# Performance work log

Measured on AMD Instinct MI355X. Metric: run time of the kernel, lower is better.

## Reference

```python
import jax, jax.numpy as jnp
import numpy as np

N_NODES = 100000
N_EDGES = 1600000
DIM = 64
N_GRAPHS = 1000


def setup_inputs() -> dict:
    key = jax.random.key(0)
    ks = jax.random.split(key, 6)
    s = 1.0 / np.sqrt(DIM)
    x = jax.random.normal(ks[0], (N_NODES, DIM), dtype=jnp.float32)
    edge_index = jax.random.randint(ks[1], (2, N_EDGES), 0, N_NODES, dtype=jnp.int64)
    batch = jnp.sort(jax.random.randint(ks[2], (N_NODES,), 0, N_GRAPHS, dtype=jnp.int64))
    W1 = jax.random.normal(ks[3], (DIM, DIM), dtype=jnp.float32) * s
    b1 = jnp.zeros((DIM,), jnp.float32)
    W2 = jax.random.normal(ks[4], (DIM, DIM), dtype=jnp.float32) * s
    b2 = jnp.zeros((DIM,), jnp.float32)
    return {"x": x, "W1": W1, "b1": b1, "W2": W2, "b2": b2,
            "edge_index": edge_index, "batch": batch}


def reference(x, W1, b1, W2, b2, edge_index, batch):
    n = x.shape[0]
    loop = jnp.arange(n, dtype=edge_index.dtype)
    src = jnp.concatenate([edge_index[0], loop])  # [E+N] with self-loops
    dst = jnp.concatenate([edge_index[1], loop])
    # symmetric GCN normalization: deg^{-1/2}[src] * deg^{-1/2}[dst]
    deg = jax.ops.segment_sum(jnp.ones(src.shape[0], x.dtype), dst, num_segments=n)
    dinv = jax.lax.rsqrt(jnp.maximum(deg, 1.0))  # deg >= 1 due to self-loops
    norm = (dinv[src] * dinv[dst])[:, None]      # [E+N, 1]

    def gcn(h, W, b):
        h = h @ W                                  # transform first (smaller dim path)
        msg = h[src] * norm                        # gather + normalize
        return jax.ops.segment_sum(msg, dst, num_segments=n) + b

    h = jax.nn.relu(gcn(x, W1, b1))
    # dropout: eval mode -> identity
    h = jax.nn.relu(gcn(h, W2, b2))

    counts = jax.ops.segment_sum(jnp.ones((n,), x.dtype), batch, num_segments=N_GRAPHS)
    pooled = jax.ops.segment_sum(h, batch, num_segments=N_GRAPHS)
    return pooled / jnp.maximum(counts, 1.0)[:, None]
```

## Files before the change

kernel.cpp:

```cpp
#include <hip/hip_runtime.h>
#include <hip/hip_fp16.h>

#define DIM 64
#define BIN_SHIFT 7
#define BINSZ 128
#define MAXBINS 1024
#define PB 512
#define PB_LOG 9

typedef __attribute__((ext_vector_type(2))) float floatx2;
typedef __attribute__((ext_vector_type(4))) float f32x4;
typedef __attribute__((ext_vector_type(8))) _Float16 f16x8;
typedef __attribute__((ext_vector_type(4))) _Float16 f16x4;

__device__ __forceinline__ int slice_of(int bid) {
    return ((bid & 7) << 6) | (bid >> 3);
}

__device__ __forceinline__ void scan_bsums(const int* __restrict__ bsums, int nb2,
                                           int* __restrict__ bp) {
    int t = threadIdx.x;
    if (t < 64) {
        int a = (t < nb2) ? bsums[t] : 0;
        int b = (64 + t < nb2) ? bsums[64 + t] : 0;
        int A = a, B = b;
#pragma unroll
        for (int d = 1; d < 64; d <<= 1) {
            int ta = __shfl_up(A, d); if (t >= d) A += ta;
            int tb = __shfl_up(B, d); if (t >= d) B += tb;
        }
        int Ta = __shfl(A, 63);
        bp[t] = A - a;
        bp[64 + t] = Ta + B - b;
    }
}


__global__ __launch_bounds__(256) void k_hist(const int* __restrict__ dst,
                                              int* __restrict__ C, int E, int NB) {
    __shared__ int h[MAXBINS];
    for (int i = threadIdx.x; i < NB; i += 256) h[i] = 0;
    __syncthreads();
    int blk = slice_of(blockIdx.x);
    int per = (E + PB - 1) / PB;
    int e0 = blk * per;
    int e1 = e0 + per; if (e1 > E) e1 = E;
    for (int e = e0 + (int)threadIdx.x; e < e1; e += 256)
        atomicAdd(&h[dst[e] >> BIN_SHIFT], 1);
    __syncthreads();
    for (int i = threadIdx.x; i < NB; i += 256)
        C[i * PB + blk] = h[i];
}


__global__ __launch_bounds__(1024) void k_scanA(const int* __restrict__ C,
                                                int* __restrict__ S,
                                                int* __restrict__ bsums, int M) {
    __shared__ int sh[1024];
    int tid = threadIdx.x;
    int j0 = blockIdx.x * 4096 + tid * 4;
    int v[4]; int sum = 0;
#pragma unroll
    for (int t = 0; t < 4; ++t) {
        int j = j0 + t;
        int x = (j < M) ? C[j] : 0;
        v[t] = sum; sum += x;
    }
    sh[tid] = sum;
    __syncthreads();
#pragma unroll
    for (int d = 1; d < 1024; d <<= 1) {
        int t = (tid >= d) ? sh[tid - d] : 0;
        __syncthreads();
        sh[tid] += t;
        __syncthreads();
    }
    int excl = sh[tid] - sum;
#pragma unroll
    for (int t = 0; t < 4; ++t) {
        int j = j0 + t;
        if (j < M) S[j] = excl + v[t];
    }
    if (tid == 1023) bsums[blockIdx.x] = sh[1023];
}


__global__ __launch_bounds__(256) void k_bucket(const int* __restrict__ src,
                                                const int* __restrict__ dst,
                                                const int* __restrict__ S,
                                                const int* __restrict__ bsums,
                                                int* __restrict__ bkt, int E, int NB,
                                                int nb2) {
    __shared__ int lcur[MAXBINS];
    __shared__ int bp[128];
    scan_bsums(bsums, nb2, bp);
    int blk = slice_of(blockIdx.x);
    __syncthreads();
    for (int i = threadIdx.x; i < NB; i += 256) {
        int j = i * PB + blk;
        lcur[i] = S[j] + bp[j >> 12];
    }
    __syncthreads();
    int per = (E + PB - 1) / PB;
    int e0 = blk * per;
    int e1 = e0 + per; if (e1 > E) e1 = E;
    for (int e = e0 + (int)threadIdx.x; e < e1; e += 256) {
        int d = dst[e];
        int pos = atomicAdd(&lcur[d >> BIN_SHIFT], 1);
        bkt[pos] = src[e] | ((d & (BINSZ - 1)) << 24);
    }
}


__global__ __launch_bounds__(256) void k_binsort(const int* __restrict__ bkt,
                                                 const int* __restrict__ S,
                                                 const int* __restrict__ bsums,
                                                 int* __restrict__ csr,
                                                 int* __restrict__ off,
                                                 float* __restrict__ dinv,
                                                 const int* __restrict__ batch,
                                                 int* __restrict__ goff,
                                                 float* __restrict__ outz,
                                                 int N, int G, int E, int NB, int nb2) {
    __shared__ int cnt[BINSZ], bas[BINSZ], cur[BINSZ];
    __shared__ int wsum[4];
    __shared__ int bp[128];
    int tid = threadIdx.x;
    int b = blockIdx.x;
    scan_bsums(bsums, nb2, bp);
    if (tid < BINSZ) { cnt[tid] = 0; cur[tid] = 0; }
    for (int i = b * 256 + tid; i < G * DIM; i += NB * 256) outz[i] = 0.f;
    __syncthreads();
    int j0 = b << PB_LOG;
    int s0 = S[j0] + bp[j0 >> 12];
    int s1 = E;
    if (b + 1 < NB) { int j1 = (b + 1) << PB_LOG; s1 = S[j1] + bp[j1 >> 12]; }
    for (int i = s0 + tid; i < s1; i += 256)
        atomicAdd(&cnt[(bkt[i] >> 24) & (BINSZ - 1)], 1);
    __syncthreads();
    int my = (tid < BINSZ) ? cnt[tid] : 0;
    int lane = tid & 63, wv = tid >> 6;
    int x = my;
#pragma unroll
    for (int d = 1; d < 64; d <<= 1) {
        int t = __shfl_up(x, d);
        if (lane >= d) x += t;
    }
    if (lane == 63) wsum[wv] = x;
    __syncthreads();
    int prefix = 0;
    for (int w = 0; w < wv; ++w) prefix += wsum[w];
    int ex = x + prefix - my;
    if (tid < BINSZ) {
        bas[tid] = ex;
        int v = (b << BIN_SHIFT) + tid;
        if (v < N) {
            off[v] = s0 + ex;
            dinv[v] = rsqrtf((float)(my + 1));
            if (v == N - 1) off[N] = E;
            int bb = batch[v];
            int prev = (v == 0) ? -1 : batch[v - 1];
            for (int g = prev + 1; g <= bb; ++g) goff[g] = v;
            if (v == N - 1)
                for (int g = bb + 1; g <= G; ++g) goff[g] = N;
        }
    }
    __syncthreads();
    for (int i = s0 + tid; i < s1; i += 256) {
        int p = bkt[i];
        int lo = (p >> 24) & (BINSZ - 1);
        int li = atomicAdd(&cur[lo], 1);
        csr[s0 + bas[lo] + li] = p & 0xFFFFFF;
    }
}


__global__ __launch_bounds__(256) void k_gemm(const float* __restrict__ X,
                                              const float* __restrict__ W,
                                              const float* __restrict__ dinv,
                                              unsigned int* __restrict__ Y8, int N) {
    __shared__ float Os[16 * 68];
    int tid = threadIdx.x;
    int lane = tid & 63, w = tid >> 6;
    int m = lane & 15, g = lane >> 4;
    int row0 = blockIdx.x * 16;
    int row = row0 + m;

    f16x8 B0, B1;
    {
        int n = (w << 4) + m;
        const float* wp = W + (g << 3) * 64 + n;
#pragma unroll
        for (int j = 0; j < 8; ++j) B0[j] = (_Float16)wp[j * 64];
        wp += 32 * 64;
#pragma unroll
        for (int j = 0; j < 8; ++j) B1[j] = (_Float16)wp[j * 64];
    }
    f16x8 A0, A1;
    {
        float4 u0 = make_float4(0.f, 0.f, 0.f, 0.f), u1 = u0, u2 = u0, u3 = u0;
        if (row < N) {
            const float* xp = X + (size_t)row * DIM + (g << 3);
            u0 = *(const float4*)(xp);
            u1 = *(const float4*)(xp + 4);
            u2 = *(const float4*)(xp + 32);
            u3 = *(const float4*)(xp + 36);
        }
        A0[0] = (_Float16)u0.x; A0[1] = (_Float16)u0.y; A0[2] = (_Float16)u0.z; A0[3] = (_Float16)u0.w;
        A0[4] = (_Float16)u1.x; A0[5] = (_Float16)u1.y; A0[6] = (_Float16)u1.z; A0[7] = (_Float16)u1.w;
        A1[0] = (_Float16)u2.x; A1[1] = (_Float16)u2.y; A1[2] = (_Float16)u2.z; A1[3] = (_Float16)u2.w;
        A1[4] = (_Float16)u3.x; A1[5] = (_Float16)u3.y; A1[6] = (_Float16)u3.z; A1[7] = (_Float16)u3.w;
    }
    f32x4 acc = {0.f, 0.f, 0.f, 0.f};
    acc = __builtin_amdgcn_mfma_f32_16x16x32_f16(A0, B0, acc, 0, 0, 0);
    acc = __builtin_amdgcn_mfma_f32_16x16x32_f16(A1, B1, acc, 0, 0, 0);
#pragma unroll
    for (int j = 0; j < 4; ++j)
        Os[((g << 2) + j) * 68 + (w << 4) + m] = acc[j];
    __syncthreads();

    int r = tid >> 4, c = tid & 15;
    int orow = row0 + r;
    if (orow < N) {
        float4 o = *(const float4*)(Os + r * 68 + (c << 2));
        float s = dinv[orow];
        int p = 0;
        p = __builtin_amdgcn_cvt_pk_fp8_f32(o.x * s, o.y * s, p, false);
        p = __builtin_amdgcn_cvt_pk_fp8_f32(o.z * s, o.w * s, p, true);
        Y8[(size_t)orow * 16 + c] = (unsigned int)p;
    } else if (orow == N) {
        Y8[(size_t)orow * 16 + c] = 0u;
    }
}


__device__ __forceinline__ float4 gather_rows(const unsigned int* __restrict__ hs8,
                                              const int* __restrict__ csr,
                                              int k0, int k1, int v, int l, int gw4,
                                              int N) {
    float4 a0, a1, a2, a3;
    {
        unsigned int u = hs8[(unsigned)((v << 4) | l)];
        floatx2 f0 = __builtin_amdgcn_cvt_pk_f32_fp8((int)u, false);
        floatx2 f1 = __builtin_amdgcn_cvt_pk_f32_fp8((int)u, true);
        a0 = make_float4(f0.x, f0.y, f1.x, f1.y);
        a1 = make_float4(0.f, 0.f, 0.f, 0.f);
        a2 = make_float4(0.f, 0.f, 0.f, 0.f);
        a3 = make_float4(0.f, 0.f, 0.f, 0.f);
    }
    for (int kb = k0; kb < k1; kb += 16) {
        int rem = k1 - kb;
        int idx = (l < rem) ? csr[kb + l] : N;
        unsigned uu[16];
#pragma unroll
        for (int t = 0; t < 16; ++t) {
            int s = __shfl(idx, gw4 + t);
            uu[t] = hs8[(unsigned)((s << 4) | l)];
        }
#pragma unroll
        for (int t = 0; t < 16; t += 4) {
            floatx2 q0 = __builtin_amdgcn_cvt_pk_f32_fp8((int)uu[t + 0], false);
            floatx2 q1 = __builtin_amdgcn_cvt_pk_f32_fp8((int)uu[t + 0], true);
            floatx2 q2 = __builtin_amdgcn_cvt_pk_f32_fp8((int)uu[t + 1], false);
            floatx2 q3 = __builtin_amdgcn_cvt_pk_f32_fp8((int)uu[t + 1], true);
            floatx2 q4 = __builtin_amdgcn_cvt_pk_f32_fp8((int)uu[t + 2], false);
            floatx2 q5 = __builtin_amdgcn_cvt_pk_f32_fp8((int)uu[t + 2], true);
            floatx2 q6 = __builtin_amdgcn_cvt_pk_f32_fp8((int)uu[t + 3], false);
            floatx2 q7 = __builtin_amdgcn_cvt_pk_f32_fp8((int)uu[t + 3], true);
            a0.x += q0.x; a0.y += q0.y; a0.z += q1.x; a0.w += q1.y;
            a1.x += q2.x; a1.y += q2.y; a1.z += q3.x; a1.w += q3.y;
            a2.x += q4.x; a2.y += q4.y; a2.z += q5.x; a2.w += q5.y;
            a3.x += q6.x; a3.y += q6.y; a3.z += q7.x; a3.w += q7.y;
        }
    }
    return make_float4(a0.x + a1.x + a2.x + a3.x,
                       a0.y + a1.y + a2.y + a3.y,
                       a0.z + a1.z + a2.z + a3.z,
                       a0.w + a1.w + a2.w + a3.w);
}


__global__ __launch_bounds__(256) void k_gather_gemm(const unsigned int* __restrict__ hs8,
                                                     const int* __restrict__ csr,
                                                     const int* __restrict__ off,
                                                     const float* __restrict__ dinv,
                                                     const float* __restrict__ bias,
                                                     const float* __restrict__ W,
                                                     unsigned int* __restrict__ hs_out,
                                                     int N) {
    __shared__ _Float16 Xs[16 * 72];
    __shared__ float Os[16 * 68];
    int tid = threadIdx.x;
    int r = tid >> 4, l = tid & 15;
    int lane = tid & 63, w = tid >> 6;
    int m = lane & 15, g = lane >> 4;
    int gw4 = (r & 3) << 4;
    int v = blockIdx.x * 16 + r;

    f16x8 B0, B1;
    {
        int n = (w << 4) + m;
        const float* wp = W + (g << 3) * 64 + n;
#pragma unroll
        for (int j = 0; j < 8; ++j) B0[j] = (_Float16)wp[j * 64];
        wp += 32 * 64;
#pragma unroll
        for (int j = 0; j < 8; ++j) B1[j] = (_Float16)wp[j * 64];
    }
    if (blockIdx.x == 0 && tid < 16)
        hs_out[(size_t)N * 16 + tid] = 0u;

    float dv = 0.f;
    float4 h = make_float4(0.f, 0.f, 0.f, 0.f);
    if (v < N) {
        dv = dinv[v];
        float4 bv = ((const float4*)bias)[l];
        float4 acc = gather_rows(hs8, csr, off[v], off[v + 1], v, l, gw4, N);
        h.x = fmaxf(acc.x * dv + bv.x, 0.f);
        h.y = fmaxf(acc.y * dv + bv.y, 0.f);
        h.z = fmaxf(acc.z * dv + bv.z, 0.f);
        h.w = fmaxf(acc.w * dv + bv.w, 0.f);
    }
    {
        f16x4 hv;
        hv[0] = (_Float16)h.x; hv[1] = (_Float16)h.y;
        hv[2] = (_Float16)h.z; hv[3] = (_Float16)h.w;
        *(f16x4*)(Xs + r * 72 + (l << 2)) = hv;
    }
    __syncthreads();

    f16x8 A0 = *(const f16x8*)(Xs + m * 72 + (g << 3));
    f16x8 A1 = *(const f16x8*)(Xs + m * 72 + 32 + (g << 3));
    f32x4 acc2 = {0.f, 0.f, 0.f, 0.f};
    acc2 = __builtin_amdgcn_mfma_f32_16x16x32_f16(A0, B0, acc2, 0, 0, 0);
    acc2 = __builtin_amdgcn_mfma_f32_16x16x32_f16(A1, B1, acc2, 0, 0, 0);
#pragma unroll
    for (int j = 0; j < 4; ++j)
        Os[((g << 2) + j) * 68 + (w << 4) + m] = acc2[j];
    __syncthreads();

    if (v < N) {
        float4 o = *(const float4*)(Os + r * 68 + (l << 2));
        int p = 0;
        p = __builtin_amdgcn_cvt_pk_fp8_f32(o.x * dv, o.y * dv, p, false);
        p = __builtin_amdgcn_cvt_pk_fp8_f32(o.z * dv, o.w * dv, p, true);
        hs_out[(size_t)v * 16 + l] = (unsigned int)p;
    }
}


__global__ __launch_bounds__(256) void k_gather_pool(const unsigned int* __restrict__ hs8,
                                                     const int* __restrict__ csr,
                                                     const int* __restrict__ off,
                                                     const float* __restrict__ dinv,
                                                     const float* __restrict__ bias,
                                                     const int* __restrict__ batch,
                                                     const int* __restrict__ goff,
                                                     float* __restrict__ out, int N) {
    __shared__ float vals[16][68];
    __shared__ int gid[16];
    int tid = threadIdx.x;
    int r = tid >> 4, l = tid & 15;
    int gw4 = (r & 3) << 4;
    int v = blockIdx.x * 16 + r;

    float4 val = make_float4(0.f, 0.f, 0.f, 0.f);
    int g = -1;
    if (v < N) {
        g = batch[v];
        float dv = dinv[v];
        float4 bv = ((const float4*)bias)[l];
        float4 acc = gather_rows(hs8, csr, off[v], off[v + 1], v, l, gw4, N);
        float inv = 1.0f / (float)(goff[g + 1] - goff[g]);
        val.x = fmaxf(acc.x * dv + bv.x, 0.f) * inv;
        val.y = fmaxf(acc.y * dv + bv.y, 0.f) * inv;
        val.z = fmaxf(acc.z * dv + bv.z, 0.f) * inv;
        val.w = fmaxf(acc.w * dv + bv.w, 0.f) * inv;
    }
    *(float4*)(&vals[r][l << 2]) = val;
    if (l == 0) gid[r] = g;
    __syncthreads();

    if (v < N) {
        bool leader = (r == 0) || (gid[r - 1] != g);
        if (leader) {
            float4 sacc = val;
            for (int rr = r + 1; rr < 16 && gid[rr] == g; ++rr) {
                float4 t = *(const float4*)(&vals[rr][l << 2]);
                sacc.x += t.x; sacc.y += t.y; sacc.z += t.z; sacc.w += t.w;
            }
            float* op = out + (size_t)g * DIM + (l << 2);
            atomicAdd(op + 0, sacc.x);
            atomicAdd(op + 1, sacc.y);
            atomicAdd(op + 2, sacc.z);
            atomicAdd(op + 3, sacc.w);
        }
    }
}


static inline int cdiv(int a, int b) { return (a + b - 1) / b; }

extern "C" void kernel_launch(void* const* d_in, const int* in_sizes, int n_in,
                              void* d_out, int out_size, void* d_ws, size_t ws_size,
                              hipStream_t stream) {
    const float* x   = (const float*)d_in[0];
    const float* W1  = (const float*)d_in[1];
    const float* b1  = (const float*)d_in[2];
    const float* W2  = (const float*)d_in[3];
    const float* b2  = (const float*)d_in[4];
    const int*   ei  = (const int*)d_in[5];
    const int*   bat = (const int*)d_in[6];

    const int N = in_sizes[0] / DIM;
    const int E = in_sizes[5] / 2;
    const int G = out_size / DIM;
    const int NB = cdiv(N, BINSZ);
    const int M  = NB * PB;
    const int* src = ei;
    const int* dst = ei + E;
    float* out = (float*)d_out;

    __half* hs1    = (__half*)d_ws;
    __half* hs2    = hs1 + (size_t)(N + 1) * DIM;
    float*  dinv   = (float*)(hs2 + (size_t)(N + 1) * DIM);
    int*    off    = (int*)(dinv + N);
    int*    goff   = off + (N + 1);
    int*    C      = goff + (G + 1);
    int*    S      = C + (size_t)PB * NB;
    int*    bsums  = S + (size_t)PB * NB;
    int*    csr    = bsums + 1024;
    int*    bkt    = (int*)hs1;

    int nb2 = cdiv(M, 4096);

    k_hist<<<PB, 256, 0, stream>>>(dst, C, E, NB);
    k_scanA<<<nb2, 1024, 0, stream>>>(C, S, bsums, M);
    k_bucket<<<PB, 256, 0, stream>>>(src, dst, S, bsums, bkt, E, NB, nb2);
    k_binsort<<<NB, 256, 0, stream>>>(bkt, S, bsums, csr, off, dinv, bat, goff,
                                      out, N, G, E, NB, nb2);

    k_gemm<<<cdiv(N + 1, 16), 256, 0, stream>>>(x, W1, dinv, (unsigned int*)hs1, N);

    k_gather_gemm<<<cdiv(N, 16), 256, 0, stream>>>((const unsigned int*)hs1, csr, off,
                                                   dinv, b1, W2, (unsigned int*)hs2, N);

    k_gather_pool<<<cdiv(N, 16), 256, 0, stream>>>((const unsigned int*)hs2, csr, off,
                                                   dinv, b2, bat, goff, out, N);
}
```

Baseline: 187.6 us.

## Fuse CSR preprocessing kernels into one cooperative kernel with grid syncs

Merges the histogram, scan, bucket and bin-sort kernels into a single cooperative kernel of 512 blocks that uses grid-wide barriers between phases. The scan is re-chunked to 1024 elements per block so the block sums fit in a 512-entry local scan, and the bin-sort phase loops over bins with a grid-stride. This removes three kernel launch gaps. In exchange it pays grid-sync overhead, and the bin-sort phase now runs on 512 persistent blocks instead of one block per bin.

```diff
diff --git a/kernel.cpp b/kernel.cpp
--- a/kernel.cpp
+++ b/kernel.cpp
@@ -1,5 +1,8 @@
 #include <hip/hip_runtime.h>
 #include <hip/hip_fp16.h>
+#include <hip/hip_cooperative_groups.h>
+
+namespace cg = cooperative_groups;
 
 #define DIM 64
 #define BIN_SHIFT 7
@@ -17,160 +20,147 @@
     return ((bid & 7) << 6) | (bid >> 3);
 }
 
-__device__ __forceinline__ void scan_bsums(const int* __restrict__ bsums, int nb2,
-                                           int* __restrict__ bp) {
-    int t = threadIdx.x;
-    if (t < 64) {
-        int a = (t < nb2) ? bsums[t] : 0;
-        int b = (64 + t < nb2) ? bsums[64 + t] : 0;
-        int A = a, B = b;
-#pragma unroll
-        for (int d = 1; d < 64; d <<= 1) {
-            int ta = __shfl_up(A, d); if (t >= d) A += ta;
-            int tb = __shfl_up(B, d); if (t >= d) B += tb;
-        }
-        int Ta = __shfl(A, 63);
-        bp[t] = A - a;
-        bp[64 + t] = Ta + B - b;
-    }
-}
-
-
-__global__ __launch_bounds__(256) void k_hist(const int* __restrict__ dst,
-                                              int* __restrict__ C, int E, int NB) {
-    __shared__ int h[MAXBINS];
-    for (int i = threadIdx.x; i < NB; i += 256) h[i] = 0;
-    __syncthreads();
-    int blk = slice_of(blockIdx.x);
+
+__global__ __launch_bounds__(256, 2) void k_pre(const int* __restrict__ src,
+                                                const int* __restrict__ dst,
+                                                int* __restrict__ C,
+                                                int* __restrict__ S,
+                                                int* __restrict__ bsums,
+                                                int* __restrict__ bkt,
+                                                int* __restrict__ csr,
+                                                int* __restrict__ off,
+                                                float* __restrict__ dinv,
+                                                const int* __restrict__ batch,
+                                                int* __restrict__ goff,
+                                                float* __restrict__ outz,
+                                                int N, int G, int E, int NB, int nch) {
+    cg::grid_group grid = cg::this_grid();
+    __shared__ int sh[MAXBINS];
+    __shared__ int bp[512];
+    __shared__ int wsum[4];
+    int tid = threadIdx.x;
+    int bid = blockIdx.x;
+    int blk = slice_of(bid);
     int per = (E + PB - 1) / PB;
     int e0 = blk * per;
     int e1 = e0 + per; if (e1 > E) e1 = E;
-    for (int e = e0 + (int)threadIdx.x; e < e1; e += 256)
-        atomicAdd(&h[dst[e] >> BIN_SHIFT], 1);
-    __syncthreads();
-    for (int i = threadIdx.x; i < NB; i += 256)
-        C[i * PB + blk] = h[i];
-}
-
-
-__global__ __launch_bounds__(1024) void k_scanA(const int* __restrict__ C,
-                                                int* __restrict__ S,
-                                                int* __restrict__ bsums, int M) {
-    __shared__ int sh[1024];
-    int tid = threadIdx.x;
-    int j0 = blockIdx.x * 4096 + tid * 4;
-    int v[4]; int sum = 0;
-#pragma unroll
-    for (int t = 0; t < 4; ++t) {
-        int j = j0 + t;
-        int x = (j < M) ? C[j] : 0;
-        v[t] = sum; sum += x;
-    }
-    sh[tid] = sum;
-    __syncthreads();
-#pragma unroll
-    for (int d = 1; d < 1024; d <<= 1) {
-        int t = (tid >= d) ? sh[tid - d] : 0;
-        __syncthreads();
-        sh[tid] += t;
-        __syncthreads();
-    }
-    int excl = sh[tid] - sum;
-#pragma unroll
-    for (int t = 0; t < 4; ++t) {
-        int j = j0 + t;
-        if (j < M) S[j] = excl + v[t];
-    }
-    if (tid == 1023) bsums[blockIdx.x] = sh[1023];
-}
-
-
-__global__ __launch_bounds__(256) void k_bucket(const int* __restrict__ src,
-                                                const int* __restrict__ dst,
-                                                const int* __restrict__ S,
-                                                const int* __restrict__ bsums,
-                                                int* __restrict__ bkt, int E, int NB,
-                                                int nb2) {
-    __shared__ int lcur[MAXBINS];
-    __shared__ int bp[128];
-    scan_bsums(bsums, nb2, bp);
-    int blk = slice_of(blockIdx.x);
-    __syncthreads();
-    for (int i = threadIdx.x; i < NB; i += 256) {
+    int M = NB * PB;
+
+    for (int i = tid; i < NB; i += 256) sh[i] = 0;
+    __syncthreads();
+    for (int e = e0 + tid; e < e1; e += 256)
+        atomicAdd(&sh[dst[e] >> BIN_SHIFT], 1);
+    __syncthreads();
+    for (int i = tid; i < NB; i += 256)
+        C[i * PB + blk] = sh[i];
+    for (int i = bid * 256 + tid; i < G * DIM; i += PB * 256) outz[i] = 0.f;
+    grid.sync();
+
+    if (bid < nch) {
+        int j0 = bid * 1024 + tid * 4;
+        int v[4]; int sum = 0;
+#pragma unroll
+        for (int t = 0; t < 4; ++t) {
+            int j = j0 + t;
+            int x = (j < M) ? C[j] : 0;
+            v[t] = sum; sum += x;
+        }
+        sh[tid] = sum;
+        __syncthreads();
+#pragma unroll
+        for (int d = 1; d < 256; d <<= 1) {
+            int t = (tid >= d) ? sh[tid - d] : 0;
+            __syncthreads();
+            sh[tid] += t;
+            __syncthreads();
+        }
+        int excl = sh[tid] - sum;
+#pragma unroll
+        for (int t = 0; t < 4; ++t) {
+            int j = j0 + t;
+            if (j < M) S[j] = excl + v[t];
+        }
+        if (tid == 255) bsums[bid] = sh[255];
+    }
+    grid.sync();
+
+    if (tid < 64) {
+        int v8[8]; int s = 0;
+#pragma unroll
+        for (int k = 0; k < 8; ++k) {
+            int j = tid * 8 + k;
+            v8[k] = s;
+            s += (j < nch) ? bsums[j] : 0;
+        }
+        int x = s;
+#pragma unroll
+        for (int d = 1; d < 64; d <<= 1) {
+            int t = __shfl_up(x, d);
+            if (tid >= d) x += t;
+        }
+        int base = x - s;
+#pragma unroll
+        for (int k = 0; k < 8; ++k) bp[tid * 8 + k] = base + v8[k];
+    }
+    __syncthreads();
+    for (int i = tid; i < NB; i += 256) {
         int j = i * PB + blk;
-        lcur[i] = S[j] + bp[j >> 12];
-    }
-    __syncthreads();
-    int per = (E + PB - 1) / PB;
-    int e0 = blk * per;
-    int e1 = e0 + per; if (e1 > E) e1 = E;
-    for (int e = e0 + (int)threadIdx.x; e < e1; e += 256) {
+        sh[i] = S[j] + bp[j >> 10];
+    }
+    __syncthreads();
+    for (int e = e0 + tid; e < e1; e += 256) {
         int d = dst[e];
-        int pos = atomicAdd(&lcur[d >> BIN_SHIFT], 1);
+        int pos = atomicAdd(&sh[d >> BIN_SHIFT], 1);
         bkt[pos] = src[e] | ((d & (BINSZ - 1)) << 24);
     }
-}
-
-
-__global__ __launch_bounds__(256) void k_binsort(const int* __restrict__ bkt,
-                                                 const int* __restrict__ S,
-                                                 const int* __restrict__ bsums,
-                                                 int* __restrict__ csr,
-                                                 int* __restrict__ off,
-                                                 float* __restrict__ dinv,
-                                                 const int* __restrict__ batch,
-                                                 int* __restrict__ goff,
-                                                 float* __restrict__ outz,
-                                                 int N, int G, int E, int NB, int nb2) {
-    __shared__ int cnt[BINSZ], bas[BINSZ], cur[BINSZ];
-    __shared__ int wsum[4];
-    __shared__ int bp[128];
-    int tid = threadIdx.x;
-    int b = blockIdx.x;
-    scan_bsums(bsums, nb2, bp);
-    if (tid < BINSZ) { cnt[tid] = 0; cur[tid] = 0; }
-    for (int i = b * 256 + tid; i < G * DIM; i += NB * 256) outz[i] = 0.f;
-    __syncthreads();
-    int j0 = b << PB_LOG;
-    int s0 = S[j0] + bp[j0 >> 12];
-    int s1 = E;
-    if (b + 1 < NB) { int j1 = (b + 1) << PB_LOG; s1 = S[j1] + bp[j1 >> 12]; }
-    for (int i = s0 + tid; i < s1; i += 256)
-        atomicAdd(&cnt[(bkt[i] >> 24) & (BINSZ - 1)], 1);
-    __syncthreads();
-    int my = (tid < BINSZ) ? cnt[tid] : 0;
-    int lane = tid & 63, wv = tid >> 6;
-    int x = my;
-#pragma unroll
-    for (int d = 1; d < 64; d <<= 1) {
-        int t = __shfl_up(x, d);
-        if (lane >= d) x += t;
-    }
-    if (lane == 63) wsum[wv] = x;
-    __syncthreads();
-    int prefix = 0;
-    for (int w = 0; w < wv; ++w) prefix += wsum[w];
-    int ex = x + prefix - my;
-    if (tid < BINSZ) {
-        bas[tid] = ex;
-        int v = (b << BIN_SHIFT) + tid;
-        if (v < N) {
-            off[v] = s0 + ex;
-            dinv[v] = rsqrtf((float)(my + 1));
-            if (v == N - 1) off[N] = E;
-            int bb = batch[v];
-            int prev = (v == 0) ? -1 : batch[v - 1];
-            for (int g = prev + 1; g <= bb; ++g) goff[g] = v;
-            if (v == N - 1)
-                for (int g = bb + 1; g <= G; ++g) goff[g] = N;
-        }
-    }
-    __syncthreads();
-    for (int i = s0 + tid; i < s1; i += 256) {
-        int p = bkt[i];
-        int lo = (p >> 24) & (BINSZ - 1);
-        int li = atomicAdd(&cur[lo], 1);
-        csr[s0 + bas[lo] + li] = p & 0xFFFFFF;
+    grid.sync();
+
+    int* cnt = sh; int* bas = sh + 128; int* cur = sh + 256;
+    for (int b = bid; b < NB; b += PB) {
+        int j0b = b << PB_LOG;
+        int s0 = S[j0b] + bp[j0b >> 10];
+        int s1 = E;
+        if (b + 1 < NB) { int j1 = (b + 1) << PB_LOG; s1 = S[j1] + bp[j1 >> 10]; }
+        if (tid < BINSZ) { cnt[tid] = 0; cur[tid] = 0; }
+        __syncthreads();
+        for (int i = s0 + tid; i < s1; i += 256)
+            atomicAdd(&cnt[(bkt[i] >> 24) & (BINSZ - 1)], 1);
+        __syncthreads();
+        int my = (tid < BINSZ) ? cnt[tid] : 0;
+        int lane = tid & 63, wv = tid >> 6;
+        int x = my;
+#pragma unroll
+        for (int d = 1; d < 64; d <<= 1) {
+            int t = __shfl_up(x, d);
+            if (lane >= d) x += t;
+        }
+        if (lane == 63) wsum[wv] = x;
+        __syncthreads();
+        int prefix = 0;
+        for (int w = 0; w < wv; ++w) prefix += wsum[w];
+        int ex = x + prefix - my;
+        if (tid < BINSZ) {
+            bas[tid] = ex;
+            int v = (b << BIN_SHIFT) + tid;
+            if (v < N) {
+                off[v] = s0 + ex;
+                dinv[v] = rsqrtf((float)(my + 1));
+                if (v == N - 1) off[N] = E;
+                int bb = batch[v];
+                int prev = (v == 0) ? -1 : batch[v - 1];
+                for (int g = prev + 1; g <= bb; ++g) goff[g] = v;
+                if (v == N - 1)
+                    for (int g = bb + 1; g <= G; ++g) goff[g] = N;
+            }
+        }
+        __syncthreads();
+        for (int i = s0 + tid; i < s1; i += 256) {
+            int p = bkt[i];
+            int lo = (p >> 24) & (BINSZ - 1);
+            int li = atomicAdd(&cur[lo], 1);
+            csr[s0 + bas[lo] + li] = p & 0xFFFFFF;
+        }
+        __syncthreads();
     }
 }
 
@@ -432,13 +422,16 @@
     int*    csr    = bsums + 1024;
     int*    bkt    = (int*)hs1;
 
-    int nb2 = cdiv(M, 4096);
-
-    k_hist<<<PB, 256, 0, stream>>>(dst, C, E, NB);
-    k_scanA<<<nb2, 1024, 0, stream>>>(C, S, bsums, M);
-    k_bucket<<<PB, 256, 0, stream>>>(src, dst, S, bsums, bkt, E, NB, nb2);
-    k_binsort<<<NB, 256, 0, stream>>>(bkt, S, bsums, csr, off, dinv, bat, goff,
-                                      out, N, G, E, NB, nb2);
+    int nch = (M + 1023) >> 10;
+
+    {
+        int N_ = N, G_ = G, E_ = E, NB_ = NB, nch_ = nch;
+        void* args[] = {(void*)&src, (void*)&dst, (void*)&C, (void*)&S,
+                        (void*)&bsums, (void*)&bkt, (void*)&csr, (void*)&off,
+                        (void*)&dinv, (void*)&bat, (void*)&goff, (void*)&out,
+                        (void*)&N_, (void*)&G_, (void*)&E_, (void*)&NB_, (void*)&nch_};
+        hipLaunchCooperativeKernel((void*)k_pre, dim3(PB), dim3(256), args, 0, stream);
+    }
 
     k_gemm<<<cdiv(N + 1, 16), 256, 0, stream>>>(x, W1, dinv, (unsigned int*)hs1, N);
 
```

After: 391.6 us. +108.8%, slower.
